# Kernel tuning notes

Hardware: AMD Instinct MI355X
Metric: run time of the kernel (lower is better)

Reference implementation:

```python
import jax, jax.numpy as jnp
import numpy as np

N = 100000
E = 1600000
IN_C, HID_C, OUT_C = 128, 64, 32


def _add_self_loops(edge_index, n):
    loops = jnp.arange(n, dtype=edge_index.dtype)
    src = jnp.concatenate([edge_index[0], loops])
    dst = jnp.concatenate([edge_index[1], loops])
    return src, dst


def _gcn_norm(src, dst, n):
    # symmetric normalization on A + I with unit edge weights
    deg = jax.ops.segment_sum(jnp.ones_like(dst, dtype=jnp.float32), dst, num_segments=n)
    dinv = jnp.where(deg > 0, jax.lax.rsqrt(deg), 0.0)
    return dinv[src] * dinv[dst]  # [E+N]


def _gcn_conv(x, src, dst, norm, W, b, n):
    h = x @ W                              # [N, out]
    msg = h[src] * norm[:, None]           # [E+N, out]  (dominant gather)
    out = jax.ops.segment_sum(msg, dst, num_segments=n)
    return out + b


def setup_inputs() -> dict:
    key = jax.random.key(0)
    k = jax.random.split(key, 6)
    x = jax.random.normal(k[0], (N, IN_C), dtype=jnp.float32)
    edge_index = jax.random.randint(k[1], (2, E), 0, N, dtype=jnp.int32)
    # Glorot-style init for GCN weights
    W1 = jax.random.normal(k[2], (IN_C, HID_C), dtype=jnp.float32) / np.sqrt(IN_C)
    b1 = jnp.zeros((HID_C,), dtype=jnp.float32)
    W2 = jax.random.normal(k[3], (HID_C, OUT_C), dtype=jnp.float32) / np.sqrt(HID_C)
    b2 = jnp.zeros((OUT_C,), dtype=jnp.float32)
    return {"x": x, "edge_index": edge_index, "W1": W1, "b1": b1, "W2": W2, "b2": b2}


def reference(x, edge_index, W1, b1, W2, b2):
    src, dst = _add_self_loops(edge_index, N)
    norm = _gcn_norm(src, dst, N)
    h = _gcn_conv(x, src, dst, norm, W1, b1, N)
    h = jax.nn.relu(h)
    # dropout p=0.2 is identity in eval mode
    out = _gcn_conv(h, src, dst, norm, W2, b2, N)
    return out
```

## Files before the change

kernel.cpp:

```cpp
#include <hip/hip_runtime.h>
#include <hip/hip_fp16.h>

#define N_NODES 100000
#define E_EDGES 1600000
#define IN_C 128
#define HID_C 64
#define OUT_C 32
#define BNODES 64
#define NBUCK ((N_NODES + BNODES - 1) / BNODES)
#define MAXB 2048
#define NCHUNK 256
#define CHUNK_E (E_EDGES / NCHUNK)

__device__ __forceinline__ int chunk_of_block(int b) { return (b & 7) * (NCHUNK / 8) + (b >> 3); }

__global__ void zero_gcur_kernel(int* __restrict__ gcur) {
    int i = blockIdx.x * 256 + threadIdx.x;
    if (i < NBUCK) gcur[i] = 0;
}

__global__ __launch_bounds__(1024) void bucket_scatter_kernel(const int* __restrict__ src,
                                                              const int* __restrict__ dst,
                                                              int* __restrict__ gcur,
                                                              unsigned* __restrict__ pairs) {
    __shared__ int h[NBUCK];
    for (int i = threadIdx.x; i < NBUCK; i += 1024) h[i] = 0;
    __syncthreads();
    const int chunk = chunk_of_block(blockIdx.x);
    const int base = chunk * CHUNK_E;
    int dc[7];
    int nj = 0;
    for (int j = threadIdx.x; j < CHUNK_E; j += 1024) {
        int d = dst[base + j];
        dc[nj++] = d;
        atomicAdd(&h[d >> 6], 1);
    }
    __syncthreads();
    for (int i = threadIdx.x; i < NBUCK; i += 1024) {
        int c = h[i];
        if (c > 0) h[i] = atomicAdd(&gcur[i], c);
    }
    __syncthreads();
    nj = 0;
    for (int j = threadIdx.x; j < CHUNK_E; j += 1024) {
        int d = dc[nj++];
        int pos = atomicAdd(&h[d >> 6], 1);
        pairs[(unsigned)(d >> 6) * MAXB + (unsigned)pos] =
            ((unsigned)src[base + j] << 6) | (unsigned)(d & 63);
    }
}

__global__ __launch_bounds__(256) void bucket_sort_kernel(const int* __restrict__ gcur,
                                                          unsigned* __restrict__ pairs,
                                                          int* __restrict__ row_beg,
                                                          int* __restrict__ row_end,
                                                          float* __restrict__ dinv) {
    __shared__ unsigned sp[MAXB];
    __shared__ int hcnt[BNODES], scn[BNODES], cur[BNODES];
    const int b = blockIdx.x;
    const int beg = b * MAXB;
    int cnt = gcur[b];
    if (cnt > MAXB) cnt = MAXB;
    if (threadIdx.x < BNODES) hcnt[threadIdx.x] = 0;
    __syncthreads();
    for (int j = threadIdx.x; j < cnt; j += 256) {
        unsigned p = pairs[beg + j];
        sp[j] = p;
        atomicAdd(&hcnt[p & 63], 1);
    }
    __syncthreads();
    if (threadIdx.x < BNODES) scn[threadIdx.x] = hcnt[threadIdx.x];
    __syncthreads();
    for (int off = 1; off < BNODES; off <<= 1) {
        int t = 0;
        if (threadIdx.x < BNODES && threadIdx.x >= off) t = scn[threadIdx.x - off];
        __syncthreads();
        if (threadIdx.x < BNODES) scn[threadIdx.x] += t;
        __syncthreads();
    }
    if (threadIdx.x < BNODES) {
        int ex = scn[threadIdx.x] - hcnt[threadIdx.x];
        cur[threadIdx.x] = ex;
        int node = b * BNODES + threadIdx.x;
        if (node < N_NODES) {
            row_beg[node] = beg + ex;
            row_end[node] = beg + ex + hcnt[threadIdx.x];
            dinv[node] = rsqrtf((float)hcnt[threadIdx.x] + 1.0f);
        }
    }
    __syncthreads();
    for (int j = threadIdx.x; j < cnt; j += 256) {
        unsigned p = sp[j];
        int pos = atomicAdd(&cur[p & 63], 1);
        pairs[beg + pos] = p >> 6;
    }
}

__global__ __launch_bounds__(256) void gemm1_kernel(const float* __restrict__ x,
                                                    const float* __restrict__ W1,
                                                    const float* __restrict__ dinv,
                                                    __half* __restrict__ hs) {
    __shared__ float xt[128 * 36];
    __shared__ float sWc[32 * 64];
    const int row0 = blockIdx.x * 128;
    const int colg = (threadIdx.x & 7) * 8;
    const int rowg = (threadIdx.x >> 3) * 4;
    float acc[4][8];
#pragma unroll
    for (int r = 0; r < 4; ++r)
#pragma unroll
        for (int c = 0; c < 8; ++c) acc[r][c] = 0.f;

    const float4* x4 = (const float4*)x;
    const float4* w4 = (const float4*)W1;

    for (int c = 0; c < 4; ++c) {
        __syncthreads();
#pragma unroll
        for (int i = 0; i < 4; ++i) {
            int g = i * 256 + threadIdx.x;
            int r = g >> 3, k4 = g & 7;
            int rg = min(row0 + r, N_NODES - 1);
            float4 v = x4[(size_t)rg * (IN_C / 4) + c * 8 + k4];
            *(float4*)(xt + r * 36 + k4 * 4) = v;
        }
#pragma unroll
        for (int i = 0; i < 2; ++i) {
            int f = i * 256 + threadIdx.x;
            int wr = f >> 4, wc4 = f & 15;
            *(float4*)(sWc + wr * 64 + wc4 * 4) = w4[(size_t)(c * 32 + wr) * 16 + wc4];
        }
        __syncthreads();
#pragma unroll
        for (int k4 = 0; k4 < 8; ++k4) {
            float4 xr[4];
#pragma unroll
            for (int ri = 0; ri < 4; ++ri)
                xr[ri] = *(const float4*)(xt + (rowg + ri) * 36 + k4 * 4);
#pragma unroll
            for (int j = 0; j < 4; ++j) {
                const float4* wp = (const float4*)(sWc + (k4 * 4 + j) * 64 + colg);
                float4 w0 = wp[0], w1 = wp[1];
                float wv[8] = {w0.x, w0.y, w0.z, w0.w, w1.x, w1.y, w1.z, w1.w};
#pragma unroll
                for (int ri = 0; ri < 4; ++ri) {
                    const float* xf = (const float*)&xr[ri];
                    float xs = xf[j];
#pragma unroll
                    for (int cc = 0; cc < 8; ++cc)
                        acc[ri][cc] = fmaf(xs, wv[cc], acc[ri][cc]);
                }
            }
        }
    }
#pragma unroll
    for (int ri = 0; ri < 4; ++ri) {
        int row = row0 + rowg + ri;
        if (row < N_NODES) {
            float dv = dinv[row];
            union { float4 f; __half2 h[4]; } u;
#pragma unroll
            for (int q = 0; q < 4; ++q)
                u.h[q] = __floats2half2_rn(acc[ri][2 * q] * dv, acc[ri][2 * q + 1] * dv);
            *(float4*)(hs + (size_t)row * HID_C + colg) = u.f;
        }
    }
}

__global__ __launch_bounds__(256) void agg1_kernel(const int* __restrict__ row_beg,
                                                   const int* __restrict__ row_end,
                                                   const int* __restrict__ col,
                                                   const float2* __restrict__ hsf,
                                                   const float* __restrict__ dinv,
                                                   const float* __restrict__ b1,
                                                   const float* __restrict__ W2,
                                                   __half* __restrict__ gs) {
    __shared__ float sW[HID_C * OUT_C];
    __shared__ __half2 sh2[16][HID_C / 2];
    for (int i = threadIdx.x; i < HID_C * OUT_C; i += 256) sW[i] = W2[i];

    const int nl = threadIdx.x >> 4;
    const int node = blockIdx.x * 16 + nl;
    const int lane = threadIdx.x & 15;
    const int beg = row_beg[node], end = row_end[node];
    float2 u = hsf[(size_t)node * 16 + lane];
    __half2* uh = (__half2*)&u;
    float2 t0 = __half22float2(uh[0]), t1 = __half22float2(uh[1]);
    float a0 = t0.x, a1 = t0.y, a2 = t1.x, a3 = t1.y;

    int j = beg;
    int idx0 = j + (lane & 7);
    int cv = (idx0 < end) ? col[idx0] : 0;
    while (j + 8 <= end) {
        int jn = j + 8;
        int idxn = jn + (lane & 7);
        int cvn = (idxn < end) ? col[idxn] : 0;
        int s[8];
#pragma unroll
        for (int e = 0; e < 8; ++e) s[e] = __shfl(cv, e, 8);
        float2 v[8];
#pragma unroll
        for (int e = 0; e < 8; ++e) v[e] = hsf[(size_t)s[e] * 16 + lane];
        cv = cvn;
#pragma unroll
        for (int e = 0; e < 8; ++e) {
            __half2* vh = (__half2*)&v[e];
            float2 w0 = __half22float2(vh[0]), w1 = __half22float2(vh[1]);
            a0 += w0.x; a1 += w0.y; a2 += w1.x; a3 += w1.y;
        }
        j = jn;
    }
    const int tail = end - j;
    for (int e = 0; e < tail; ++e) {
        int s = __shfl(cv, e, 8);
        float2 v = hsf[(size_t)s * 16 + lane];
        __half2* vh = (__half2*)&v;
        float2 w0 = __half22float2(vh[0]), w1 = __half22float2(vh[1]);
        a0 += w0.x; a1 += w0.y; a2 += w1.x; a3 += w1.y;
    }
    const float dv = dinv[node];
    float4 bb = ((const float4*)b1)[lane];
    __half2 p0 = __floats2half2_rn(fmaxf(dv * a0 + bb.x, 0.f), fmaxf(dv * a1 + bb.y, 0.f));
    __half2 p1 = __floats2half2_rn(fmaxf(dv * a2 + bb.z, 0.f), fmaxf(dv * a3 + bb.w, 0.f));
    sh2[nl][lane * 2] = p0;
    sh2[nl][lane * 2 + 1] = p1;
    __syncthreads();

    const int oc = lane * 2;
    float o0 = 0.f, o1 = 0.f;
#pragma unroll
    for (int k2 = 0; k2 < HID_C / 2; ++k2) {
        float2 hv = __half22float2(sh2[nl][k2]);
        const float* w0 = sW + (2 * k2) * OUT_C + oc;
        const float* w1 = sW + (2 * k2 + 1) * OUT_C + oc;
        o0 = fmaf(hv.x, w0[0], o0); o1 = fmaf(hv.x, w0[1], o1);
        o0 = fmaf(hv.y, w1[0], o0); o1 = fmaf(hv.y, w1[1], o1);
    }
    *(__half2*)(gs + (size_t)node * OUT_C + oc) = __floats2half2_rn(o0 * dv, o1 * dv);
}

__global__ void agg2_kernel(const int* __restrict__ row_beg, const int* __restrict__ row_end,
                            const int* __restrict__ col,
                            const float2* __restrict__ gsf, const float* __restrict__ dinv,
                            const float* __restrict__ b2, float* __restrict__ out) {
    const int node = blockIdx.x * 32 + (threadIdx.x >> 3);
    const int lane = threadIdx.x & 7;
    if (node >= N_NODES) return;
    const int beg = row_beg[node], end = row_end[node];
    float2 u = gsf[(size_t)node * 8 + lane];
    __half2* uh = (__half2*)&u;
    float2 t0 = __half22float2(uh[0]), t1 = __half22float2(uh[1]);
    float a0 = t0.x, a1 = t0.y, a2 = t1.x, a3 = t1.y;

    int j = beg;
    int idx0 = j + lane;
    int cv = (idx0 < end) ? col[idx0] : 0;
    while (j + 8 <= end) {
        int jn = j + 8;
        int idxn = jn + lane;
        int cvn = (idxn < end) ? col[idxn] : 0;
        int s[8];
#pragma unroll
        for (int e = 0; e < 8; ++e) s[e] = __shfl(cv, e, 8);
        float2 v[8];
#pragma unroll
        for (int e = 0; e < 8; ++e) v[e] = gsf[(size_t)s[e] * 8 + lane];
        cv = cvn;
#pragma unroll
        for (int e = 0; e < 8; ++e) {
            __half2* vh = (__half2*)&v[e];
            float2 w0 = __half22float2(vh[0]), w1 = __half22float2(vh[1]);
            a0 += w0.x; a1 += w0.y; a2 += w1.x; a3 += w1.y;
        }
        j = jn;
    }
    const int tail = end - j;
    for (int e = 0; e < tail; ++e) {
        int s = __shfl(cv, e, 8);
        float2 v = gsf[(size_t)s * 8 + lane];
        __half2* vh = (__half2*)&v;
        float2 w0 = __half22float2(vh[0]), w1 = __half22float2(vh[1]);
        a0 += w0.x; a1 += w0.y; a2 += w1.x; a3 += w1.y;
    }
    float dv = dinv[node];
    float4 bb = ((const float4*)b2)[lane];
    float4 o;
    o.x = dv * a0 + bb.x;
    o.y = dv * a1 + bb.y;
    o.z = dv * a2 + bb.z;
    o.w = dv * a3 + bb.w;
    *(float4*)(out + (size_t)node * OUT_C + lane * 4) = o;
}

extern "C" void kernel_launch(void* const* d_in, const int* in_sizes, int n_in,
                              void* d_out, int out_size, void* d_ws, size_t ws_size,
                              hipStream_t stream) {
    const float* x  = (const float*)d_in[0];
    const int*   ei = (const int*)d_in[1];
    const float* W1 = (const float*)d_in[2];
    const float* b1 = (const float*)d_in[3];
    const float* W2 = (const float*)d_in[4];
    const float* b2 = (const float*)d_in[5];
    float* out = (float*)d_out;

    const int* srcv = ei;
    const int* dstv = ei + E_EDGES;

    float* dinv  = (float*)d_ws;
    __half* hs   = (__half*)(dinv + N_NODES);
    __half* gs   = hs + (size_t)N_NODES * HID_C;
    int* row_beg = (int*)(gs + (size_t)N_NODES * OUT_C);
    int* row_end = row_beg + N_NODES;
    int* gcur    = row_end + N_NODES;
    unsigned* pairs = (unsigned*)(gcur + 1568);
    int* col = (int*)pairs;

    zero_gcur_kernel<<<(NBUCK + 255) / 256, 256, 0, stream>>>(gcur);
    bucket_scatter_kernel<<<NCHUNK, 1024, 0, stream>>>(srcv, dstv, gcur, pairs);
    bucket_sort_kernel<<<NBUCK, 256, 0, stream>>>(gcur, pairs, row_beg, row_end, dinv);

    gemm1_kernel<<<(N_NODES + 127) / 128, 256, 0, stream>>>(x, W1, dinv, hs);

    agg1_kernel<<<N_NODES / 16, 256, 0, stream>>>(row_beg, row_end, col,
                                                  (const float2*)hs, dinv, b1, W2, gs);

    agg2_kernel<<<(N_NODES + 31) / 32, 256, 0, stream>>>(row_beg, row_end, col,
                                                         (const float2*)gs, dinv, b2, out);
}
```

Before: 126.0 us.

## Compute first GEMM with split-bf16 MFMA instead of FP32 FMA

Replaces the scalar FP32 FMA tiling in gemm1 with MFMA 16x16x32 bf16 instructions. Precision is recovered with a three-term hi/lo split (ah*bh + al*bh + ah*bl). W1 is pre-split into transposed bf16 hi/lo arrays inside the init kernel, which also zeroes the bucket counters. The GEMM is only part of a pipeline dominated by sorting and aggregation, and the new per-element half stores are less coalesced than the previous vectorized ones.

```diff
diff --git a/kernel.cpp b/kernel.cpp
--- a/kernel.cpp
+++ b/kernel.cpp
@@ -12,11 +12,31 @@
 #define NCHUNK 256
 #define CHUNK_E (E_EDGES / NCHUNK)
 
+typedef __attribute__((ext_vector_type(8))) short short8;
+typedef __attribute__((ext_vector_type(4))) float f32x4;
+
+__device__ __forceinline__ unsigned short f2bf(float f) {
+    union { float f; unsigned u; } v; v.f = f;
+    return (unsigned short)((v.u + 0x7fffu + ((v.u >> 16) & 1u)) >> 16);
+}
+__device__ __forceinline__ float bf2f(unsigned short b) {
+    union { unsigned u; float f; } v; v.u = ((unsigned)b) << 16;
+    return v.f;
+}
+
 __device__ __forceinline__ int chunk_of_block(int b) { return (b & 7) * (NCHUNK / 8) + (b >> 3); }
 
-__global__ void zero_gcur_kernel(int* __restrict__ gcur) {
+__global__ void init_kernel(int* __restrict__ gcur, const float* __restrict__ W1,
+                            unsigned short* __restrict__ WtH, unsigned short* __restrict__ WtL) {
     int i = blockIdx.x * 256 + threadIdx.x;
-    if (i < NBUCK) gcur[i] = 0;
+    if (i < 1568) gcur[i] = 0;
+    if (i < IN_C * HID_C) {
+        int k = i >> 6, c = i & 63;
+        float w = W1[i];
+        unsigned short h = f2bf(w);
+        WtH[c * IN_C + k] = h;
+        WtL[c * IN_C + k] = f2bf(w - bf2f(h));
+    }
 }
 
 __global__ __launch_bounds__(1024) void bucket_scatter_kernel(const int* __restrict__ src,
@@ -97,72 +117,63 @@
 }
 
 __global__ __launch_bounds__(256) void gemm1_kernel(const float* __restrict__ x,
-                                                    const float* __restrict__ W1,
+                                                    const unsigned short* __restrict__ WtH,
+                                                    const unsigned short* __restrict__ WtL,
                                                     const float* __restrict__ dinv,
                                                     __half* __restrict__ hs) {
-    __shared__ float xt[128 * 36];
-    __shared__ float sWc[32 * 64];
-    const int row0 = blockIdx.x * 128;
-    const int colg = (threadIdx.x & 7) * 8;
-    const int rowg = (threadIdx.x >> 3) * 4;
-    float acc[4][8];
-#pragma unroll
-    for (int r = 0; r < 4; ++r)
-#pragma unroll
-        for (int c = 0; c < 8; ++c) acc[r][c] = 0.f;
-
+    __shared__ float xt[64 * 36];
+    const int l = threadIdx.x & 63;
+    const int wv = threadIdx.x >> 6;
+    const int row0 = blockIdx.x * 64;
+    const int rA = l & 15;
+    const int kg = l >> 4;
     const float4* x4 = (const float4*)x;
-    const float4* w4 = (const float4*)W1;
-
-    for (int c = 0; c < 4; ++c) {
+
+    f32x4 acc[4];
+#pragma unroll
+    for (int n = 0; n < 4; ++n) acc[n] = (f32x4){0.f, 0.f, 0.f, 0.f};
+
+    for (int ks = 0; ks < 4; ++ks) {
         __syncthreads();
 #pragma unroll
-        for (int i = 0; i < 4; ++i) {
+        for (int i = 0; i < 2; ++i) {
             int g = i * 256 + threadIdx.x;
             int r = g >> 3, k4 = g & 7;
             int rg = min(row0 + r, N_NODES - 1);
-            float4 v = x4[(size_t)rg * (IN_C / 4) + c * 8 + k4];
+            float4 v = x4[(size_t)rg * (IN_C / 4) + ks * 8 + k4];
             *(float4*)(xt + r * 36 + k4 * 4) = v;
         }
-#pragma unroll
-        for (int i = 0; i < 2; ++i) {
-            int f = i * 256 + threadIdx.x;
-            int wr = f >> 4, wc4 = f & 15;
-            *(float4*)(sWc + wr * 64 + wc4 * 4) = w4[(size_t)(c * 32 + wr) * 16 + wc4];
-        }
         __syncthreads();
-#pragma unroll
-        for (int k4 = 0; k4 < 8; ++k4) {
-            float4 xr[4];
-#pragma unroll
-            for (int ri = 0; ri < 4; ++ri)
-                xr[ri] = *(const float4*)(xt + (rowg + ri) * 36 + k4 * 4);
-#pragma unroll
-            for (int j = 0; j < 4; ++j) {
-                const float4* wp = (const float4*)(sWc + (k4 * 4 + j) * 64 + colg);
-                float4 w0 = wp[0], w1 = wp[1];
-                float wv[8] = {w0.x, w0.y, w0.z, w0.w, w1.x, w1.y, w1.z, w1.w};
-#pragma unroll
-                for (int ri = 0; ri < 4; ++ri) {
-                    const float* xf = (const float*)&xr[ri];
-                    float xs = xf[j];
-#pragma unroll
-                    for (int cc = 0; cc < 8; ++cc)
-                        acc[ri][cc] = fmaf(xs, wv[cc], acc[ri][cc]);
-                }
-            }
-        }
-    }
-#pragma unroll
-    for (int ri = 0; ri < 4; ++ri) {
-        int row = row0 + rowg + ri;
+        const float* xp = xt + (wv * 16 + rA) * 36 + kg * 8;
+        float4 xa = *(const float4*)xp;
+        float4 xb = *(const float4*)(xp + 4);
+        float xs[8] = {xa.x, xa.y, xa.z, xa.w, xb.x, xb.y, xb.z, xb.w};
+        short8 ah, al;
+#pragma unroll
+        for (int b = 0; b < 8; ++b) {
+            unsigned short hbits = f2bf(xs[b]);
+            ah[b] = (short)hbits;
+            al[b] = (short)f2bf(xs[b] - bf2f(hbits));
+        }
+        const int kb = ks * 32 + kg * 8;
+#pragma unroll
+        for (int n = 0; n < 4; ++n) {
+            int c = n * 16 + rA;
+            short8 bh = *(const short8*)(WtH + c * IN_C + kb);
+            short8 bl = *(const short8*)(WtL + c * IN_C + kb);
+            acc[n] = __builtin_amdgcn_mfma_f32_16x16x32_bf16(ah, bh, acc[n], 0, 0, 0);
+            acc[n] = __builtin_amdgcn_mfma_f32_16x16x32_bf16(al, bh, acc[n], 0, 0, 0);
+            acc[n] = __builtin_amdgcn_mfma_f32_16x16x32_bf16(ah, bl, acc[n], 0, 0, 0);
+        }
+    }
+#pragma unroll
+    for (int j = 0; j < 4; ++j) {
+        int row = row0 + wv * 16 + kg * 4 + j;
         if (row < N_NODES) {
             float dv = dinv[row];
-            union { float4 f; __half2 h[4]; } u;
-#pragma unroll
-            for (int q = 0; q < 4; ++q)
-                u.h[q] = __floats2half2_rn(acc[ri][2 * q] * dv, acc[ri][2 * q + 1] * dv);
-            *(float4*)(hs + (size_t)row * HID_C + colg) = u.f;
+#pragma unroll
+            for (int n = 0; n < 4; ++n)
+                hs[(size_t)row * HID_C + n * 16 + rA] = __float2half(acc[n][j] * dv);
         }
     }
 }
@@ -312,14 +323,16 @@
     int* row_beg = (int*)(gs + (size_t)N_NODES * OUT_C);
     int* row_end = row_beg + N_NODES;
     int* gcur    = row_end + N_NODES;
-    unsigned* pairs = (unsigned*)(gcur + 1568);
+    unsigned short* WtH = (unsigned short*)(gcur + 1568);
+    unsigned short* WtL = WtH + IN_C * HID_C;
+    unsigned* pairs = (unsigned*)(WtL + IN_C * HID_C);
     int* col = (int*)pairs;
 
-    zero_gcur_kernel<<<(NBUCK + 255) / 256, 256, 0, stream>>>(gcur);
+    init_kernel<<<32, 256, 0, stream>>>(gcur, W1, WtH, WtL);
     bucket_scatter_kernel<<<NCHUNK, 1024, 0, stream>>>(srcv, dstv, gcur, pairs);
     bucket_sort_kernel<<<NBUCK, 256, 0, stream>>>(gcur, pairs, row_beg, row_end, dinv);
 
-    gemm1_kernel<<<(N_NODES + 127) / 128, 256, 0, stream>>>(x, W1, dinv, hs);
+    gemm1_kernel<<<(N_NODES + 63) / 64, 256, 0, stream>>>(x, WtH, WtL, dinv, hs);
 
     agg1_kernel<<<N_NODES / 16, 256, 0, stream>>>(row_beg, row_end, col,
                                                   (const float2*)hs, dinv, b1, W2, gs);
```

Result: slower. 136.9 us (+8.6%).
